# Kernel optimization log

Measured on AMD Instinct MI355X. Metric: run time of the kernel, lower is better.

## Reference

```python
import jax, jax.numpy as jnp
import numpy as np

N = 50000
NEIGH = 32
D_IN = 128
D_OUT = 128

def setup_inputs() -> dict:
    key = jax.random.key(0)
    k1, k2, k3, k4 = jax.random.split(key, 4)
    self_vecs = jax.random.normal(k1, (N, D_IN), dtype=jnp.float32)
    neigh_vecs = jax.random.normal(k2, (N * NEIGH, D_IN), dtype=jnp.float32)
    weight = jax.random.normal(k3, (D_IN, D_OUT), dtype=jnp.float32) * (1.0 / np.sqrt(D_IN))
    bias = jax.random.normal(k4, (D_OUT,), dtype=jnp.float32) * 0.01
    return {"self_vecs": self_vecs, "neigh_vecs": neigh_vecs, "neigh_num": NEIGH,
            "weight": weight, "bias": bias}

def reference(self_vecs, neigh_vecs, neigh_num, weight, bias):
    # self_h: [N, 1, F], neigh_h: [N, neigh_num, F]
    self_h = jnp.matmul(self_vecs, weight)[:, None, :]
    neigh_h = jnp.matmul(neigh_vecs, weight).reshape(-1, neigh_num, weight.shape[1])
    # concat along neighbor axis then mean == mean of (neigh_num+1) rows
    out = jnp.mean(jnp.concatenate([self_h, neigh_h], axis=1), axis=1)
    return out + bias
```

## Files before the change

kernel.cpp:

```cpp
#include <hip/hip_runtime.h>


constexpr int D       = 128;
constexpr int NEIGH   = 32;
constexpr int NPB     = 16;
constexpr int THREADS = 512;

__global__ __launch_bounds__(THREADS, 4)
void sparse_layer_fused(const float* __restrict__ self_vecs,
                        const float* __restrict__ neigh_vecs,
                        const float* __restrict__ weight,
                        const float* __restrict__ bias,
                        float* __restrict__ out)
{
    __shared__ float w_lds[D * D];
    __shared__ float agg_lds[NPB][D];

    {
        const float4* w4 = reinterpret_cast<const float4*>(weight);
        float4*       wl = reinterpret_cast<float4*>(w_lds);
        #pragma unroll
        for (int i = 0; i < (D * D / 4) / THREADS; ++i)
            wl[threadIdx.x + i * THREADS] = w4[threadIdx.x + i * THREADS];
    }

    const int  local = threadIdx.x >> 5;
    const int  c4    = threadIdx.x & 31;
    const long node  = (long)blockIdx.x * NPB + local;

    const float4* s4 = reinterpret_cast<const float4*>(self_vecs);
    const float4* n4 = reinterpret_cast<const float4*>(neigh_vecs);

    float4 acc = s4[node * (D / 4) + c4];
    const float4* nrow = n4 + node * (long)NEIGH * (D / 4) + c4;
    #pragma unroll 8
    for (int r = 0; r < NEIGH; ++r) {
        float4 v = nrow[(long)r * (D / 4)];
        acc.x += v.x; acc.y += v.y; acc.z += v.z; acc.w += v.w;
    }
    constexpr float inv = 1.0f / 33.0f;
    float4 sc;
    sc.x = acc.x * inv; sc.y = acc.y * inv; sc.z = acc.z * inv; sc.w = acc.w * inv;
    reinterpret_cast<float4*>(agg_lds[local])[c4] = sc;

    __syncthreads();

    float4 o = make_float4(0.f, 0.f, 0.f, 0.f);
    const float4* arow4 = reinterpret_cast<const float4*>(agg_lds[local]);
    #pragma unroll 4
    for (int k4 = 0; k4 < D / 4; ++k4) {
        float4 a  = arow4[k4];
        float4 w0 = reinterpret_cast<const float4*>(w_lds + (4*k4+0) * D)[c4];
        float4 w1 = reinterpret_cast<const float4*>(w_lds + (4*k4+1) * D)[c4];
        float4 w2 = reinterpret_cast<const float4*>(w_lds + (4*k4+2) * D)[c4];
        float4 w3 = reinterpret_cast<const float4*>(w_lds + (4*k4+3) * D)[c4];
        o.x += a.x * w0.x; o.y += a.x * w0.y; o.z += a.x * w0.z; o.w += a.x * w0.w;
        o.x += a.y * w1.x; o.y += a.y * w1.y; o.z += a.y * w1.z; o.w += a.y * w1.w;
        o.x += a.z * w2.x; o.y += a.z * w2.y; o.z += a.z * w2.z; o.w += a.z * w2.w;
        o.x += a.w * w3.x; o.y += a.w * w3.y; o.z += a.w * w3.z; o.w += a.w * w3.w;
    }
    float4 b = reinterpret_cast<const float4*>(bias)[c4];
    o.x += b.x; o.y += b.y; o.z += b.z; o.w += b.w;
    reinterpret_cast<float4*>(out)[node * (D / 4) + c4] = o;
}

extern "C" void kernel_launch(void* const* d_in, const int* in_sizes, int n_in,
                              void* d_out, int out_size, void* d_ws, size_t ws_size,
                              hipStream_t stream) {
    const float* self_vecs  = (const float*)d_in[0];
    const float* neigh_vecs = (const float*)d_in[1];
    const float* weight     = (const float*)d_in[3];
    const float* bias       = (const float*)d_in[4];
    float*       out        = (float*)d_out;

    const int n_nodes = in_sizes[0] / D;
    const int blocks  = n_nodes / NPB;
    hipLaunchKernelGGL(sparse_layer_fused, dim3(blocks), dim3(THREADS), 0, stream,
                       self_vecs, neigh_vecs, weight, bias, out);
}
```

Baseline: 173.8 us.

## Process four nodes per wave with split-K matvec and shuffle reductions

```diff
diff --git a/kernel.cpp b/kernel.cpp
--- a/kernel.cpp
+++ b/kernel.cpp
@@ -1,67 +1,86 @@
 #include <hip/hip_runtime.h>
 
 
+typedef float f32x4 __attribute__((ext_vector_type(4)));
+
 constexpr int D       = 128;
+constexpr int D4      = D / 4;
 constexpr int NEIGH   = 32;
-constexpr int NPB     = 16;
-constexpr int THREADS = 512;
+constexpr int WAVES   = 8;
+constexpr int THREADS = WAVES * 64;
+constexpr int NPW     = 4;
+constexpr int NPB     = WAVES * NPW;
 
 __global__ __launch_bounds__(THREADS, 4)
-void sparse_layer_fused(const float* __restrict__ self_vecs,
-                        const float* __restrict__ neigh_vecs,
-                        const float* __restrict__ weight,
-                        const float* __restrict__ bias,
-                        float* __restrict__ out)
+void sparse_layer_v3(const float* __restrict__ self_vecs,
+                     const float* __restrict__ neigh_vecs,
+                     const float* __restrict__ weight,
+                     const float* __restrict__ bias,
+                     float* __restrict__ out, int n_nodes)
 {
     __shared__ float w_lds[D * D];
-    __shared__ float agg_lds[NPB][D];
+    __shared__ float agg_lds[WAVES][D];
 
     {
-        const float4* w4 = reinterpret_cast<const float4*>(weight);
-        float4*       wl = reinterpret_cast<float4*>(w_lds);
+        const f32x4* w4 = reinterpret_cast<const f32x4*>(weight);
+        f32x4*       wp = reinterpret_cast<f32x4*>(w_lds);
         #pragma unroll
         for (int i = 0; i < (D * D / 4) / THREADS; ++i)
-            wl[threadIdx.x + i * THREADS] = w4[threadIdx.x + i * THREADS];
+            wp[threadIdx.x + i * THREADS] = w4[threadIdx.x + i * THREADS];
     }
-
-    const int  local = threadIdx.x >> 5;
-    const int  c4    = threadIdx.x & 31;
-    const long node  = (long)blockIdx.x * NPB + local;
-
-    const float4* s4 = reinterpret_cast<const float4*>(self_vecs);
-    const float4* n4 = reinterpret_cast<const float4*>(neigh_vecs);
-
-    float4 acc = s4[node * (D / 4) + c4];
-    const float4* nrow = n4 + node * (long)NEIGH * (D / 4) + c4;
-    #pragma unroll 8
-    for (int r = 0; r < NEIGH; ++r) {
-        float4 v = nrow[(long)r * (D / 4)];
-        acc.x += v.x; acc.y += v.y; acc.z += v.z; acc.w += v.w;
-    }
-    constexpr float inv = 1.0f / 33.0f;
-    float4 sc;
-    sc.x = acc.x * inv; sc.y = acc.y * inv; sc.z = acc.z * inv; sc.w = acc.w * inv;
-    reinterpret_cast<float4*>(agg_lds[local])[c4] = sc;
-
     __syncthreads();
 
-    float4 o = make_float4(0.f, 0.f, 0.f, 0.f);
-    const float4* arow4 = reinterpret_cast<const float4*>(agg_lds[local]);
-    #pragma unroll 4
-    for (int k4 = 0; k4 < D / 4; ++k4) {
-        float4 a  = arow4[k4];
-        float4 w0 = reinterpret_cast<const float4*>(w_lds + (4*k4+0) * D)[c4];
-        float4 w1 = reinterpret_cast<const float4*>(w_lds + (4*k4+1) * D)[c4];
-        float4 w2 = reinterpret_cast<const float4*>(w_lds + (4*k4+2) * D)[c4];
-        float4 w3 = reinterpret_cast<const float4*>(w_lds + (4*k4+3) * D)[c4];
-        o.x += a.x * w0.x; o.y += a.x * w0.y; o.z += a.x * w0.z; o.w += a.x * w0.w;
-        o.x += a.y * w1.x; o.y += a.y * w1.y; o.z += a.y * w1.z; o.w += a.y * w1.w;
-        o.x += a.z * w2.x; o.y += a.z * w2.y; o.z += a.z * w2.z; o.w += a.z * w2.w;
-        o.x += a.w * w3.x; o.y += a.w * w3.y; o.z += a.w * w3.z; o.w += a.w * w3.w;
+    const int wave = threadIdx.x >> 6;
+    const int lane = threadIdx.x & 63;
+    const int h    = lane >> 5;
+    const int c4   = lane & 31;
+
+    const f32x4* s4 = reinterpret_cast<const f32x4*>(self_vecs);
+    const f32x4* g4 = reinterpret_cast<const f32x4*>(neigh_vecs);
+    const f32x4* wl = reinterpret_cast<const f32x4*>(w_lds);
+    f32x4* arow = reinterpret_cast<f32x4*>(agg_lds[wave]);
+    const f32x4 bv = reinterpret_cast<const f32x4*>(bias)[c4];
+    constexpr float inv = 1.0f / (NEIGH + 1);
+
+    const long base = (long)blockIdx.x * NPB + wave * NPW;
+
+    for (int i = 0; i < NPW; ++i) {
+        const long n = base + i;
+        if (n >= n_nodes) break;
+
+        const f32x4* p = g4 + n * (long)NEIGH * D4;
+        f32x4 acc = (f32x4)0.0f;
+        if (h == 0) acc = s4[n * D4 + c4];
+        #pragma unroll
+        for (int l = 0; l < 16; ++l)
+            acc += p[l * 64 + lane];
+
+        f32x4 tot;
+        tot.x = acc.x + __shfl_xor(acc.x, 32);
+        tot.y = acc.y + __shfl_xor(acc.y, 32);
+        tot.z = acc.z + __shfl_xor(acc.z, 32);
+        tot.w = acc.w + __shfl_xor(acc.w, 32);
+        tot *= inv;
+        if (h == 0) arow[c4] = tot;
+
+        f32x4 o = (f32x4)0.0f;
+        #pragma unroll
+        for (int k4 = 0; k4 < D4 / 2; ++k4) {
+            const int kk = h * (D4 / 2) + k4;
+            f32x4 a  = arow[kk];
+            f32x4 w0 = wl[(4 * kk + 0) * D4 + c4];
+            f32x4 w1 = wl[(4 * kk + 1) * D4 + c4];
+            f32x4 w2 = wl[(4 * kk + 2) * D4 + c4];
+            f32x4 w3 = wl[(4 * kk + 3) * D4 + c4];
+            o += a.x * w0;  o += a.y * w1;  o += a.z * w2;  o += a.w * w3;
+        }
+        o.x += __shfl_xor(o.x, 32);
+        o.y += __shfl_xor(o.y, 32);
+        o.z += __shfl_xor(o.z, 32);
+        o.w += __shfl_xor(o.w, 32);
+        if (h == 0)
+            reinterpret_cast<f32x4*>(out)[n * D4 + c4] = o + bv;
     }
-    float4 b = reinterpret_cast<const float4*>(bias)[c4];
-    o.x += b.x; o.y += b.y; o.z += b.z; o.w += b.w;
-    reinterpret_cast<float4*>(out)[node * (D / 4) + c4] = o;
 }
 
 extern "C" void kernel_launch(void* const* d_in, const int* in_sizes, int n_in,
@@ -74,7 +93,7 @@
     float*       out        = (float*)d_out;
 
     const int n_nodes = in_sizes[0] / D;
-    const int blocks  = n_nodes / NPB;
-    hipLaunchKernelGGL(sparse_layer_fused, dim3(blocks), dim3(THREADS), 0, stream,
-                       self_vecs, neigh_vecs, weight, bias, out);
+    const int blocks  = (n_nodes + NPB - 1) / NPB;
+    hipLaunchKernelGGL(sparse_layer_v3, dim3(blocks), dim3(THREADS), 0, stream,
+                       self_vecs, neigh_vecs, weight, bias, out, n_nodes);
 }
```

Result: slower. 178.6 us (+2.7%).
